# Optimization experiments

Hardware: AMD Instinct MI355X
Metric: run time of the kernel (lower is better)

The kernel has to match this reference:

```python
import jax, jax.numpy as jnp
import numpy as np

H = 1024   # hidden_dim
I = 256    # input_dim
T = 128    # time_step
NW = 4     # input_num (weeks)
N = 100    # stocks = 5 categories * 20
C, G = 5, 20


def gru(x, Wih, Whh, bih, bhh):
    """Torch-style single-layer GRU. x: (B,T,I) batch_first -> (B,T,H). Gate order r,z,n."""
    gx = jnp.einsum('bti,gi->btg', x, Wih) + bih  # (B,T,3H) input projections precomputed
    h0 = jnp.zeros((x.shape[0], Whh.shape[1]), x.dtype)

    def step(h, g):
        gh = h @ Whh.T + bhh
        xr, xz, xn = jnp.split(g, 3, axis=-1)
        hr, hz, hn = jnp.split(gh, 3, axis=-1)
        r = jax.nn.sigmoid(xr + hr)
        z = jax.nn.sigmoid(xz + hz)
        n = jnp.tanh(xn + r * hn)
        h = (1.0 - z) * n + z * h
        return h, h

    _, ys = jax.lax.scan(step, h0, jnp.swapaxes(gx, 0, 1))
    return jnp.swapaxes(ys, 0, 1)


def att_block(x, W, b):
    """AttentionBlock: x (B,T,D); Linear over time axis, softmax over time, weighted sum."""
    xt = jnp.swapaxes(x, 1, 2)                    # (B,D,T)
    probs = jax.nn.softmax(xt @ W.T + b, axis=-1) # (B,D,T)
    probs = jnp.swapaxes(probs, 1, 2)             # (B,T,D)
    return (probs * x).sum(axis=1)                # (B,D)


def gat(x, edges, W, a_s, a_d, bias):
    """PyG GATConv, heads=1, add_self_loops=True, leaky_relu slope 0.2."""
    n = x.shape[0]
    h = x @ W.T                                   # (n,H)
    loop = jnp.arange(n)
    src = jnp.concatenate([edges[0], loop])
    dst = jnp.concatenate([edges[1], loop])
    e = jax.nn.leaky_relu((h @ a_s)[src] + (h @ a_d)[dst], 0.2)
    m = jax.ops.segment_max(e, dst, num_segments=n)
    ex = jnp.exp(e - m[dst])
    s = jax.ops.segment_sum(ex, dst, num_segments=n)
    alpha = ex / s[dst]
    return jax.ops.segment_sum(alpha[:, None] * h[src], dst, num_segments=n) + bias


def setup_inputs() -> dict:
    key = jax.random.key(0)
    ks = iter(jax.random.split(key, 64))
    p = lambda *s: jax.random.normal(next(ks), s, dtype=jnp.float32) * 0.05
    inp = {}
    for i in range(NW):
        inp[f'w{i}'] = jax.random.normal(next(ks), (N, T, I), dtype=jnp.float32)
    inp['inner_edge'] = jax.random.randint(next(ks), (2, 2000), 0, N, dtype=jnp.int32)
    inp['outer_edge'] = jax.random.randint(next(ks), (2, 25), 0, C, dtype=jnp.int32)
    # per-week sequence encoders (stacked)
    inp['enc_Wih'] = p(NW, 3 * H, I); inp['enc_Whh'] = p(NW, 3 * H, H)
    inp['enc_bih'] = p(NW, 3 * H);    inp['enc_bhh'] = p(NW, 3 * H)
    inp['enc_attW'] = p(NW, T, T);    inp['enc_attb'] = p(NW, T)
    # weekly GRU (not batch_first in torch!)
    inp['wk_Wih'] = p(3 * H, H); inp['wk_Whh'] = p(3 * H, H)
    inp['wk_bih'] = p(3 * H);    inp['wk_bhh'] = p(3 * H)
    inp['wkatt_W'] = p(NW, NW); inp['wkatt_b'] = p(NW)
    inp['pool_W'] = p(G, G);    inp['pool_b'] = p(G)
    inp['ig_W'] = p(H, H); inp['ig_as'] = p(H); inp['ig_ad'] = p(H); inp['ig_b'] = p(H)
    inp['cg_W'] = p(H, H); inp['cg_as'] = p(H); inp['cg_ad'] = p(H); inp['cg_b'] = p(H)
    inp['fus_W'] = p(H, 3 * H); inp['fus_b'] = p(H)
    inp['reg_W'] = p(1, H); inp['reg_b'] = p(1)
    inp['cls_W'] = p(1, H); inp['cls_b'] = p(1)
    return inp


def reference(w0, w1, w2, w3, inner_edge, outer_edge,
              enc_Wih, enc_Whh, enc_bih, enc_bhh, enc_attW, enc_attb,
              wk_Wih, wk_Whh, wk_bih, wk_bhh, wkatt_W, wkatt_b,
              pool_W, pool_b, ig_W, ig_as, ig_ad, ig_b,
              cg_W, cg_as, cg_ad, cg_b, fus_W, fus_b,
              reg_W, reg_b, cls_W, cls_b):
    weeks = [w0, w1, w2, w3]
    embs = []
    for i in range(NW):
        seq = gru(weeks[i], enc_Wih[i], enc_Whh[i], enc_bih[i], enc_bhh[i])  # (N,T,H)
        embs.append(att_block(seq, enc_attW[i], enc_attb[i])[:, None, :])    # (N,1,H)
    we = jnp.concatenate(embs, axis=1)                                       # (N,NW,H)
    # torch nn.GRU default seq-major: scans over dim0 (N stocks), batch=NW
    we = jnp.swapaxes(gru(jnp.swapaxes(we, 0, 1), wk_Wih, wk_Whh, wk_bih, wk_bhh), 0, 1)
    wav = att_block(we, wkatt_W, wkatt_b)                                    # (N,H)
    inner = gat(wav, inner_edge, ig_W, ig_as, ig_ad, ig_b).reshape(C, G, -1)
    wav3 = wav.reshape(C, G, -1)
    cat = att_block(wav3, pool_W, pool_b)                                    # (C,H)
    cat = gat(cat, outer_edge, cg_W, cg_as, cg_ad, cg_b)                     # (C,H)
    cat = jnp.broadcast_to(cat[:, None, :], (C, G, cat.shape[-1]))
    f = jnp.concatenate([wav3, cat, inner], axis=-1)                         # (C,G,3H)
    f = jax.nn.relu(f @ fus_W.T + fus_b)
    reg = (f @ reg_W.T + reg_b).reshape(-1)
    cls = jax.nn.sigmoid(f @ cls_W.T + cls_b).reshape(-1)
    return reg, cls
```

## Files before the change

kernel.cpp:

```cpp
#include <hip/hip_runtime.h>
#include <hip/hip_bf16.h>

#define NW 4
#define NST 100
#define TT 128
#define II 256
#define HH 1024
#define H3 3072

typedef _Float16 h8 __attribute__((ext_vector_type(8)));
typedef float f4 __attribute__((ext_vector_type(4)));

__device__ __forceinline__ float sigf(float x) { return 1.0f / (1.0f + expf(-x)); }

__device__ __forceinline__ float4 ld_f4_sc1(const float* p) {
    union { unsigned long long u[2]; float4 v; } r;
    r.u[0] = __hip_atomic_load((unsigned long long*)p, __ATOMIC_RELAXED, __HIP_MEMORY_SCOPE_AGENT);
    r.u[1] = __hip_atomic_load((unsigned long long*)p + 1, __ATOMIC_RELAXED, __HIP_MEMORY_SCOPE_AGENT);
    return r.v;
}
__device__ __forceinline__ float ld_f_sc1(const float* p) {
    return __hip_atomic_load((float*)p, __ATOMIC_RELAXED, __HIP_MEMORY_SCOPE_AGENT);
}

__device__ __forceinline__ void spin_wait(unsigned* f, unsigned t) {
    int guard = 0;
    while (__hip_atomic_load(f, __ATOMIC_RELAXED, __HIP_MEMORY_SCOPE_AGENT) <= t) {
        __builtin_amdgcn_s_sleep(2);
        if (++guard > (1 << 20)) break;
    }
}

__global__ void zero_k(float* a, int n) {
    int i = blockIdx.x * 256 + threadIdx.x;
    if (i < n) a[i] = 0.0f;
}

__global__ void convW_k(const float* __restrict__ Whh, const float* __restrict__ Wih,
                        _Float16* __restrict__ Wc) {
    int col = blockIdx.x * 256 + threadIdx.x;
    int r = blockIdx.y;
    int w = blockIdx.z;
    float v = (col < HH) ? Whh[((size_t)w * H3 + r) * HH + col]
                         : Wih[((size_t)w * H3 + r) * II + (col - HH)];
    Wc[((size_t)w * H3 + r) * 1280 + col] = (_Float16)v;
}

__global__ void convWk_k(const float* __restrict__ src, _Float16* __restrict__ dst) {
    int col = blockIdx.x * 256 + threadIdx.x;
    int r = blockIdx.y;
    dst[(size_t)r * HH + col] = (_Float16)src[(size_t)r * HH + col];
}

__global__ void xcvt_k(const float* __restrict__ x0, const float* __restrict__ x1,
                       const float* __restrict__ x2, const float* __restrict__ x3,
                       _Float16* __restrict__ xT) {
    int idx = blockIdx.x * 256 + threadIdx.x;
    int k8 = idx & 31;
    int m  = (idx >> 5) & 127;
    int t  = (idx >> 12) & 127;
    int w  = idx >> 19;
    const float* xw = (w == 0) ? x0 : (w == 1) ? x1 : (w == 2) ? x2 : x3;
    h8 hv = {};
    if (m < NST) {
        const float* s = xw + ((size_t)m * TT + t) * II + k8 * 8;
        float4 fa = *(const float4*)s;
        float4 fb = *(const float4*)(s + 4);
        hv[0] = (_Float16)fa.x; hv[1] = (_Float16)fa.y;
        hv[2] = (_Float16)fa.z; hv[3] = (_Float16)fa.w;
        hv[4] = (_Float16)fb.x; hv[5] = (_Float16)fb.y;
        hv[6] = (_Float16)fb.z; hv[7] = (_Float16)fb.w;
    }
    *(h8*)&xT[(((size_t)w * TT + t) * 128 + m) * II + k8 * 8] = hv;
}

__global__ void wTcvt_k(const float* __restrict__ attW, float* __restrict__ wT) {
    int tp = threadIdx.x;
    int t  = blockIdx.x;
    int w  = blockIdx.y;
    wT[((size_t)w * TT + t) * TT + tp] = attW[((size_t)w * TT + tp) * TT + t];
}

__global__ void convB_k(const float* __restrict__ bih, const float* __restrict__ bhh,
                        float* __restrict__ bc) {
    int j = blockIdx.x * 256 + threadIdx.x;
    int w = blockIdx.y;
    const float* bi = bih + w * H3;
    const float* bh = bhh + w * H3;
    float* o = bc + w * 4096;
    o[j] = bi[j] + bh[j];
    o[1024 + j] = bi[1024 + j] + bh[1024 + j];
    o[2048 + j] = bi[2048 + j];
    o[3072 + j] = bh[2048 + j];
}

#define ENC_LDS_HALFS (40 * 48 * 40)
#define ENC_LDS_BYTES (ENC_LDS_HALFS * 2)

__global__ __launch_bounds__(256) void enc_fused_k(
    const _Float16* __restrict__ Wc, const float* __restrict__ bc,
    const _Float16* __restrict__ xT,
    _Float16* __restrict__ hhA, _Float16* __restrict__ hhB,
    _Float16* __restrict__ seq, unsigned* flags)
{
    extern __shared__ _Float16 Bs[];

    int id = blockIdx.x;
    int rr = id & 7, qq = id >> 3;
    int w  = rr >> 1;
    int bx = qq * 2 + (rr & 1);
    int j0 = bx * 16;

    const _Float16* Wcw = Wc + (size_t)w * H3 * 1280;
    const float* bcw = bc + w * 4096;
    _Float16* hA = hhA + (size_t)w * 128 * HH;
    _Float16* hB = hhB + (size_t)w * 128 * HH;
    unsigned* fw = flags + (size_t)w * 64 * 16;

    int tid = threadIdx.x;
    int lane = tid & 63, wi = tid >> 6, quad = lane >> 4, l15 = lane & 15;

    if (tid < 192) {
        int brow = tid >> 2, bseg = tid & 3;
        const _Float16* bsrc =
            Wcw + (size_t)((brow >> 4) * 1024 + j0 + (brow & 15)) * 1280 + bseg * 8;
        #pragma unroll 8
        for (int c = 0; c < 40; c++) {
            uint4 v = *(const uint4*)(bsrc + c * 32);
            *(uint4*)&Bs[((size_t)c * 48 + brow) * 40 + bseg * 8] = v;
        }
    }
    __syncthreads();

    int j = j0 + l15;
    float br = bcw[j], bz = bcw[1024 + j], bni = bcw[2048 + j], bnh = bcw[3072 + j];
    int r0 = wi * 32 + l15, r1 = wi * 32 + 16 + l15;
    float hreg[2][4] = {};

    for (int t = 0; t < TT; t++) {
        const _Float16* hin = (t & 1) ? hB : hA;
        _Float16* hout = (t & 1) ? hA : hB;
        const _Float16* xt = xT + ((size_t)w * TT + t) * 128 * II;
        const _Float16* pA0h = hin + (size_t)r0 * HH + quad * 8;
        const _Float16* pA1h = hin + (size_t)r1 * HH + quad * 8;
        const _Float16* pA0x = xt + (size_t)r0 * II + quad * 8;
        const _Float16* pA1x = xt + (size_t)r1 * II + quad * 8;

        f4 aR[2] = {}, aZ[2] = {}, aNH[2] = {}, aNX[2] = {};

        h8 rb0[8], rb1[8];
        #pragma unroll
        for (int u = 0; u < 8; u++) {
            rb0[u] = *(const h8*)(pA0h + u * 32);
            rb1[u] = *(const h8*)(pA1h + u * 32);
        }

        #pragma unroll 8
        for (int c = 0; c < 40; c++) {
            int u = c & 7;
            h8 a0 = rb0[u], a1 = rb1[u];
            int cn = c + 8;
            if (cn < 32) {
                rb0[u] = *(const h8*)(pA0h + cn * 32);
                rb1[u] = *(const h8*)(pA1h + cn * 32);
            } else if (cn < 40) {
                rb0[u] = *(const h8*)(pA0x + (cn - 32) * 32);
                rb1[u] = *(const h8*)(pA1x + (cn - 32) * 32);
            }
            const _Float16* bb = &Bs[(size_t)(c * 48) * 40];
            h8 bf0 = *(const h8*)&bb[l15 * 40 + quad * 8];
            h8 bf1 = *(const h8*)&bb[(16 + l15) * 40 + quad * 8];
            h8 bf2 = *(const h8*)&bb[(32 + l15) * 40 + quad * 8];
            aR[0] = __builtin_amdgcn_mfma_f32_16x16x32_f16(a0, bf0, aR[0], 0, 0, 0);
            aR[1] = __builtin_amdgcn_mfma_f32_16x16x32_f16(a1, bf0, aR[1], 0, 0, 0);
            aZ[0] = __builtin_amdgcn_mfma_f32_16x16x32_f16(a0, bf1, aZ[0], 0, 0, 0);
            aZ[1] = __builtin_amdgcn_mfma_f32_16x16x32_f16(a1, bf1, aZ[1], 0, 0, 0);
            if (c < 32) {
                aNH[0] = __builtin_amdgcn_mfma_f32_16x16x32_f16(a0, bf2, aNH[0], 0, 0, 0);
                aNH[1] = __builtin_amdgcn_mfma_f32_16x16x32_f16(a1, bf2, aNH[1], 0, 0, 0);
            } else {
                aNX[0] = __builtin_amdgcn_mfma_f32_16x16x32_f16(a0, bf2, aNX[0], 0, 0, 0);
                aNX[1] = __builtin_amdgcn_mfma_f32_16x16x32_f16(a1, bf2, aNX[1], 0, 0, 0);
            }
        }

        #pragma unroll
        for (int mi = 0; mi < 2; mi++) {
            #pragma unroll
            for (int p = 0; p < 4; p++) {
                int row = wi * 32 + mi * 16 + quad * 4 + p;
                float r = sigf(aR[mi][p] + br);
                float z = sigf(aZ[mi][p] + bz);
                float n = tanhf(aNX[mi][p] + bni + r * (aNH[mi][p] + bnh));
                float hv = (1.f - z) * n + z * hreg[mi][p];
                hreg[mi][p] = hv;
                unsigned short hb = __builtin_bit_cast(unsigned short, (_Float16)hv);
                unsigned ob = __shfl_xor((unsigned)hb, 1);
                unsigned pk = (unsigned)hb | (ob << 16);
                if (!(l15 & 1)) {
                    if (t < TT - 1)
                        __hip_atomic_store((unsigned*)&hout[(size_t)row * HH + j], pk,
                                           __ATOMIC_RELAXED, __HIP_MEMORY_SCOPE_AGENT);
                    if (row < NST)
                        __hip_atomic_store(
                            (unsigned*)&seq[(((size_t)w * NST + row) * TT + t) * HH + j], pk,
                            __ATOMIC_RELAXED, __HIP_MEMORY_SCOPE_AGENT);
                }
            }
        }
        if (t < TT - 1) {
            __syncthreads();
            if (tid == 0)
                __hip_atomic_store(&fw[bx * 16], (unsigned)(t + 1),
                                   __ATOMIC_RELAXED, __HIP_MEMORY_SCOPE_AGENT);
            if (tid < 64) spin_wait(&fw[tid * 16], (unsigned)t);
            __syncthreads();
            __builtin_amdgcn_fence(__ATOMIC_ACQUIRE, "agent");
        }
    }
}

__global__ __launch_bounds__(256) void att1_k(
    const _Float16* __restrict__ seq, const float* __restrict__ wT,
    const float* __restrict__ attb, float* __restrict__ wex)
{
    int d0 = blockIdx.x * 128;
    int n  = blockIdx.y;
    int w  = blockIdx.z;
    __shared__ _Float16 S[128][128];
    __shared__ float PM[16][136];
    int tid = threadIdx.x;
    const _Float16* sp = seq + ((size_t)(w * NST + n) * TT) * HH + d0;
    for (int q = tid; q < 2048; q += 256) {
        int t = q >> 4, seg = q & 15;
        *(h8*)&S[t][seg * 8] = *(const h8*)(sp + (size_t)t * HH + seg * 8);
    }
    __syncthreads();
    int tx = tid & 15, ty = tid >> 4;
    const float* Wg = wT + (size_t)w * TT * TT;
    float acc[8][8];
    #pragma unroll
    for (int i = 0; i < 8; i++) {
        float b = attb[w * TT + ty * 8 + i];
        for (int j = 0; j < 8; j++) acc[i][j] = b;
    }
    for (int t = 0; t < 128; t++) {
        float wv[8], sv[8];
        float4 wa = *(const float4*)&Wg[(size_t)t * TT + ty * 8];
        float4 wb = *(const float4*)&Wg[(size_t)t * TT + ty * 8 + 4];
        wv[0] = wa.x; wv[1] = wa.y; wv[2] = wa.z; wv[3] = wa.w;
        wv[4] = wb.x; wv[5] = wb.y; wv[6] = wb.z; wv[7] = wb.w;
        h8 s8 = *(const h8*)&S[t][tx * 8];
        #pragma unroll
        for (int j = 0; j < 8; j++) sv[j] = (float)s8[j];
        #pragma unroll
        for (int i = 0; i < 8; i++)
            #pragma unroll
            for (int j = 0; j < 8; j++) acc[i][j] += wv[i] * sv[j];
    }
    float cmax[8], csum[8];
    #pragma unroll
    for (int j = 0; j < 8; j++) {
        float m = acc[0][j];
        for (int i = 1; i < 8; i++) m = fmaxf(m, acc[i][j]);
        PM[ty][tx * 8 + j] = m;
    }
    __syncthreads();
    #pragma unroll
    for (int j = 0; j < 8; j++) {
        float m = -1e30f;
        for (int yy = 0; yy < 16; yy++) m = fmaxf(m, PM[yy][tx * 8 + j]);
        cmax[j] = m;
    }
    __syncthreads();
    #pragma unroll
    for (int j = 0; j < 8; j++) {
        float s = 0.f;
        for (int i = 0; i < 8; i++) { acc[i][j] = expf(acc[i][j] - cmax[j]); s += acc[i][j]; }
        PM[ty][tx * 8 + j] = s;
    }
    __syncthreads();
    #pragma unroll
    for (int j = 0; j < 8; j++) {
        float s = 0.f;
        for (int yy = 0; yy < 16; yy++) s += PM[yy][tx * 8 + j];
        csum[j] = s;
    }
    __syncthreads();
    #pragma unroll
    for (int i = 0; i < 8; i++) {
        h8 s8 = *(const h8*)&S[ty * 8 + i][tx * 8];
        #pragma unroll
        for (int j = 0; j < 8; j++) {
            if (i == 0) PM[ty][tx * 8 + j] = 0.f;
            PM[ty][tx * 8 + j] += acc[i][j] * (float)s8[j];
        }
    }
    __syncthreads();
    if (ty == 0) {
        #pragma unroll
        for (int j = 0; j < 8; j++) {
            float o = 0.f;
            for (int yy = 0; yy < 16; yy++) o += PM[yy][tx * 8 + j];
            wex[((size_t)w * NST + n) * HH + d0 + tx * 8 + j] = o / csum[j];
        }
    }
}

template <int RELU>
__global__ __launch_bounds__(256) void gemm_tn_k(
    const float* __restrict__ A, const float* __restrict__ B,
    const float* __restrict__ bias, float* __restrict__ C, int M, int N, int K)
{
    int n0 = blockIdx.x * 64, m0 = blockIdx.y * 64;
    __shared__ float As[16][64], Bs[16][64];
    int tid = threadIdx.x, tx = tid & 15, ty = tid >> 4;
    float acc[4][4] = {{0.f}};
    for (int k0 = 0; k0 < K; k0 += 16) {
        __syncthreads();
        for (int q = tid; q < 1024; q += 256) {
            int kk = q & 15, r = q >> 4;
            int m = m0 + r, nn = n0 + r;
            As[kk][r] = (m < M) ? A[(size_t)m * K + k0 + kk] : 0.f;
            Bs[kk][r] = (nn < N) ? B[(size_t)nn * K + k0 + kk] : 0.f;
        }
        __syncthreads();
        #pragma unroll
        for (int kk = 0; kk < 16; kk++) {
            float4 av = *(const float4*)&As[kk][ty * 4];
            float4 bv = *(const float4*)&Bs[kk][tx * 4];
            float a[4] = {av.x, av.y, av.z, av.w};
            float b[4] = {bv.x, bv.y, bv.z, bv.w};
            #pragma unroll
            for (int r = 0; r < 4; r++)
                #pragma unroll
                for (int c = 0; c < 4; c++) acc[r][c] += a[r] * b[c];
        }
    }
    #pragma unroll
    for (int r = 0; r < 4; r++) {
        int m = m0 + ty * 4 + r;
        if (m >= M) continue;
        #pragma unroll
        for (int c = 0; c < 4; c++) {
            int nn = n0 + tx * 4 + c;
            if (nn >= N) continue;
            float v = acc[r][c] + (bias ? bias[nn] : 0.f);
            if (RELU) v = fmaxf(v, 0.f);
            C[(size_t)m * N + nn] = v;
        }
    }
}

__global__ __launch_bounds__(256) void wk_fused_k(
    const float* __restrict__ gxw, const _Float16* __restrict__ wkW,
    const float* __restrict__ bhh, float* __restrict__ hA,
    float* __restrict__ hB, float* __restrict__ we2, unsigned* flags)
{
    int tid = threadIdx.x;
    int wi = tid >> 6, lane = tid & 63;
    int j = blockIdx.x * 4 + wi;
    int k0 = lane * 16;
    float wf[3][16];
    #pragma unroll
    for (int g = 0; g < 3; g++) {
        h8 wa = *(const h8*)&wkW[(size_t)(g * HH + j) * HH + k0];
        h8 wb = *(const h8*)&wkW[(size_t)(g * HH + j) * HH + k0 + 8];
        #pragma unroll
        for (int i = 0; i < 8; i++) { wf[g][i] = (float)wa[i]; wf[g][8 + i] = (float)wb[i]; }
    }
    float b0 = bhh[j], b1 = bhh[HH + j], b2 = bhh[2 * HH + j];

    for (int t = 0; t < NST; t++) {
        const float* hin = (t & 1) ? hB : hA;
        float* hout = (t & 1) ? hA : hB;
        float acc[4][3] = {};
        #pragma unroll
        for (int b = 0; b < 4; b++) {
            float hv[16];
            #pragma unroll
            for (int s = 0; s < 4; s++) {
                float4 hq = ld_f4_sc1(&hin[b * HH + k0 + s * 4]);
                hv[s * 4] = hq.x; hv[s * 4 + 1] = hq.y;
                hv[s * 4 + 2] = hq.z; hv[s * 4 + 3] = hq.w;
            }
            #pragma unroll
            for (int g = 0; g < 3; g++)
                #pragma unroll
                for (int i = 0; i < 16; i++) acc[b][g] += wf[g][i] * hv[i];
        }
        #pragma unroll
        for (int b = 0; b < 4; b++)
            #pragma unroll
            for (int g = 0; g < 3; g++)
                for (int o = 32; o; o >>= 1) acc[b][g] += __shfl_down(acc[b][g], o);
        if (lane == 0) {
            for (int b = 0; b < 4; b++) {
                const float* gx = gxw + ((size_t)b * NST + t) * H3;
                float hr = acc[b][0] + b0;
                float hz = acc[b][1] + b1;
                float hn = acc[b][2] + b2;
                float r = sigf(gx[j] + hr);
                float z = sigf(gx[HH + j] + hz);
                float n = tanhf(gx[2 * HH + j] + r * hn);
                float hv = (1.f - z) * n + z * ld_f_sc1(&hin[b * HH + j]);
                __hip_atomic_store(&hout[b * HH + j], hv,
                                   __ATOMIC_RELAXED, __HIP_MEMORY_SCOPE_AGENT);
                we2[((size_t)t * 4 + b) * HH + j] = hv;
            }
        }
        if (t < NST - 1) {
            __syncthreads();
            if (tid == 0)
                __hip_atomic_store(&flags[blockIdx.x * 16], (unsigned)(t + 1),
                                   __ATOMIC_RELAXED, __HIP_MEMORY_SCOPE_AGENT);
            spin_wait(&flags[tid * 16], (unsigned)t);
            __syncthreads();
        }
    }
}

__global__ void wkatt_k(const float* __restrict__ we2, const float* __restrict__ W,
                        const float* __restrict__ bv, float* __restrict__ wav)
{
    int n = blockIdx.x;
    for (int d = threadIdx.x; d < HH; d += 256) {
        float v[4], l[4];
        #pragma unroll
        for (int tp = 0; tp < 4; tp++) v[tp] = we2[((size_t)n * 4 + tp) * HH + d];
        float mx = -1e30f;
        #pragma unroll
        for (int tp = 0; tp < 4; tp++) {
            float s = bv[tp];
            for (int t2 = 0; t2 < 4; t2++) s += v[t2] * W[tp * 4 + t2];
            l[tp] = s; mx = fmaxf(mx, s);
        }
        float se = 0.f, o = 0.f;
        #pragma unroll
        for (int tp = 0; tp < 4; tp++) {
            float e = expf(l[tp] - mx);
            se += e; o += e * v[tp];
        }
        wav[(size_t)n * HH + d] = o / se;
    }
}

__global__ void poolatt_k(const float* __restrict__ wav, const float* __restrict__ W,
                          const float* __restrict__ bv, float* __restrict__ cat1)
{
    int c = blockIdx.x;
    for (int d = threadIdx.x; d < HH; d += 256) {
        float v[20], l[20];
        for (int t2 = 0; t2 < 20; t2++) v[t2] = wav[((size_t)c * 20 + t2) * HH + d];
        float mx = -1e30f;
        for (int tp = 0; tp < 20; tp++) {
            float s = bv[tp];
            for (int t2 = 0; t2 < 20; t2++) s += v[t2] * W[tp * 20 + t2];
            l[tp] = s; mx = fmaxf(mx, s);
        }
        float se = 0.f, o = 0.f;
        for (int tp = 0; tp < 20; tp++) {
            float e = expf(l[tp] - mx);
            se += e; o += e * v[tp];
        }
        cat1[(size_t)c * HH + d] = o / se;
    }
}

__global__ void gat_dots_k(const float* __restrict__ h, const float* __restrict__ as_,
                           const float* __restrict__ ad_, float* __restrict__ ss,
                           float* __restrict__ sd)
{
    int i = blockIdx.x, tid = threadIdx.x;
    float s1 = 0.f, s2 = 0.f;
    for (int k = tid; k < HH; k += 256) {
        float v = h[(size_t)i * HH + k];
        s1 += v * as_[k]; s2 += v * ad_[k];
    }
    __shared__ float r1[256], r2[256];
    r1[tid] = s1; r2[tid] = s2; __syncthreads();
    for (int s = 128; s; s >>= 1) {
        if (tid < s) { r1[tid] += r1[tid + s]; r2[tid] += r2[tid + s]; }
        __syncthreads();
    }
    if (tid == 0) { ss[i] = r1[0]; sd[i] = r2[0]; }
}

#define MAXE 256
__global__ __launch_bounds__(256) void gat_agg_k(
    const float* __restrict__ hmat, const int* __restrict__ esrc,
    const int* __restrict__ edst, int nedges, const float* __restrict__ ss,
    const float* __restrict__ sd, const float* __restrict__ bias, float* __restrict__ outp)
{
    int i = blockIdx.x, tid = threadIdx.x;
    __shared__ int cnt;
    __shared__ int msrc[MAXE];
    __shared__ float mw[MAXE];
    __shared__ float inv_s;
    if (tid == 0) {
        cnt = 1; msrc[0] = i;
        float e = ss[i] + sd[i];
        mw[0] = e > 0.f ? e : 0.2f * e;
    }
    __syncthreads();
    for (int e = tid; e < nedges; e += 256) {
        if (edst[e] == i) {
            int p = atomicAdd(&cnt, 1);
            if (p < MAXE) {
                int s = esrc[e];
                msrc[p] = s;
                float v = ss[s] + sd[i];
                mw[p] = v > 0.f ? v : 0.2f * v;
            }
        }
    }
    __syncthreads();
    int m = min(cnt, MAXE);
    if (tid == 0) {
        float mx = -1e30f;
        for (int p = 0; p < m; p++) mx = fmaxf(mx, mw[p]);
        float s = 0.f;
        for (int p = 0; p < m; p++) { float e = expf(mw[p] - mx); mw[p] = e; s += e; }
        inv_s = 1.0f / s;
    }
    __syncthreads();
    for (int d = tid; d < HH; d += 256) {
        float a = 0.f;
        for (int p = 0; p < m; p++) a += mw[p] * hmat[(size_t)msrc[p] * HH + d];
        outp[(size_t)i * HH + d] = a * inv_s + bias[d];
    }
}

__global__ void concat_k(const float* __restrict__ wav, const float* __restrict__ gc,
                         const float* __restrict__ gi, float* __restrict__ cc)
{
    int row = blockIdx.x;
    int c = row / 20;
    for (int k = threadIdx.x; k < H3; k += 256) {
        float v;
        if (k < HH) v = wav[(size_t)row * HH + k];
        else if (k < 2 * HH) v = gc[(size_t)c * HH + (k - HH)];
        else v = gi[(size_t)row * HH + (k - 2 * HH)];
        cc[(size_t)row * H3 + k] = v;
    }
}

__global__ void heads_k(const float* __restrict__ f, const float* __restrict__ regW,
                        const float* __restrict__ regb, const float* __restrict__ clsW,
                        const float* __restrict__ clsb, float* __restrict__ outp)
{
    int i = blockIdx.x, tid = threadIdx.x;
    float s1 = 0.f, s2 = 0.f;
    for (int k = tid; k < HH; k += 256) {
        float v = f[(size_t)i * HH + k];
        s1 += v * regW[k]; s2 += v * clsW[k];
    }
    __shared__ float r1[256], r2[256];
    r1[tid] = s1; r2[tid] = s2; __syncthreads();
    for (int s = 128; s; s >>= 1) {
        if (tid < s) { r1[tid] += r1[tid + s]; r2[tid] += r2[tid + s]; }
        __syncthreads();
    }
    if (tid == 0) {
        outp[i] = r1[0] + regb[0];
        outp[100 + i] = sigf(r2[0] + clsb[0]);
    }
}

extern "C" void kernel_launch(void* const* d_in, const int* in_sizes, int n_in,
                              void* d_out, int out_size, void* d_ws, size_t ws_size,
                              hipStream_t stream)
{
    (void)in_sizes; (void)n_in; (void)out_size; (void)ws_size;
    const float* x0 = (const float*)d_in[0];
    const float* x1 = (const float*)d_in[1];
    const float* x2 = (const float*)d_in[2];
    const float* x3 = (const float*)d_in[3];
    const int*   ie = (const int*)d_in[4];
    const int*   oe = (const int*)d_in[5];
    const float* enc_Wih = (const float*)d_in[6];
    const float* enc_Whh = (const float*)d_in[7];
    const float* enc_bih = (const float*)d_in[8];
    const float* enc_bhh = (const float*)d_in[9];
    const float* enc_attW = (const float*)d_in[10];
    const float* enc_attb = (const float*)d_in[11];
    const float* wk_Wih = (const float*)d_in[12];
    const float* wk_Whh = (const float*)d_in[13];
    const float* wk_bih = (const float*)d_in[14];
    const float* wk_bhh = (const float*)d_in[15];
    const float* wkatt_W = (const float*)d_in[16];
    const float* wkatt_b = (const float*)d_in[17];
    const float* pool_W = (const float*)d_in[18];
    const float* pool_b = (const float*)d_in[19];
    const float* ig_W = (const float*)d_in[20];
    const float* ig_as = (const float*)d_in[21];
    const float* ig_ad = (const float*)d_in[22];
    const float* ig_b = (const float*)d_in[23];
    const float* cg_W = (const float*)d_in[24];
    const float* cg_as = (const float*)d_in[25];
    const float* cg_ad = (const float*)d_in[26];
    const float* cg_b = (const float*)d_in[27];
    const float* fus_W = (const float*)d_in[28];
    const float* fus_b = (const float*)d_in[29];
    const float* reg_W = (const float*)d_in[30];
    const float* reg_b = (const float*)d_in[31];
    const float* cls_W = (const float*)d_in[32];
    const float* cls_b = (const float*)d_in[33];
    float* outp = (float*)d_out;

    char* p = (char*)d_ws;
    auto alloc = [&](size_t bytes) { char* r = p; p += (bytes + 255) & ~(size_t)255; return (void*)r; };
    unsigned* flags = (unsigned*)alloc(2 * 256 * 16 * 4);
    _Float16* Wcat = (_Float16*)alloc((size_t)NW * H3 * 1280 * 2);
    float* bc = (float*)alloc((size_t)NW * 4 * HH * 4);
    _Float16* wkW = (_Float16*)alloc((size_t)H3 * HH * 2);
    _Float16* xT = (_Float16*)alloc((size_t)NW * TT * 128 * II * 2);
    float* wT = (float*)alloc((size_t)NW * TT * TT * 4);
    _Float16* hhA = (_Float16*)alloc((size_t)NW * 128 * HH * 2);
    _Float16* hhB = (_Float16*)alloc((size_t)NW * 128 * HH * 2);
    _Float16* seq = (_Float16*)alloc((size_t)NW * NST * TT * HH * 2);
    float* wex = (float*)alloc((size_t)NW * NST * HH * 4);
    float* gxw = (float*)alloc((size_t)NW * NST * H3 * 4);
    float* hwA = (float*)alloc(4 * HH * 4);
    float* hwB = (float*)alloc(4 * HH * 4);
    float* we2 = (float*)alloc((size_t)NST * 4 * HH * 4);
    float* wav = (float*)alloc((size_t)NST * HH * 4);
    float* hi  = (float*)alloc((size_t)NST * HH * 4);
    float* si_s = (float*)alloc(128 * 4);
    float* si_d = (float*)alloc(128 * 4);
    float* gi  = (float*)alloc((size_t)NST * HH * 4);
    float* cat1 = (float*)alloc(5 * HH * 4);
    float* hc  = (float*)alloc(5 * HH * 4);
    float* sc_s = (float*)alloc(64 * 4);
    float* sc_d = (float*)alloc(64 * 4);
    float* gc  = (float*)alloc(5 * HH * 4);
    float* cc  = (float*)alloc((size_t)NST * H3 * 4);
    float* fbuf = (float*)alloc((size_t)NST * HH * 4);

    static bool attr_done = false;
    if (!attr_done) {
        hipFuncSetAttribute((const void*)enc_fused_k,
                            hipFuncAttributeMaxDynamicSharedMemorySize, ENC_LDS_BYTES);
        attr_done = true;
    }

    zero_k<<<32, 256, 0, stream>>>((float*)flags, 2 * 256 * 16);
    convW_k<<<dim3(5, H3, NW), 256, 0, stream>>>(enc_Whh, enc_Wih, Wcat);
    convB_k<<<dim3(4, NW), 256, 0, stream>>>(enc_bih, enc_bhh, bc);
    convWk_k<<<dim3(4, H3), 256, 0, stream>>>(wk_Whh, wkW);
    xcvt_k<<<8192, 256, 0, stream>>>(x0, x1, x2, x3, xT);
    wTcvt_k<<<dim3(TT, NW), 128, 0, stream>>>(enc_attW, wT);
    zero_k<<<(NW * 128 * HH / 2 + 255) / 256, 256, 0, stream>>>((float*)hhA, NW * 128 * HH / 2);
    zero_k<<<(4 * HH + 255) / 256, 256, 0, stream>>>(hwA, 4 * HH);

    enc_fused_k<<<256, 256, ENC_LDS_BYTES, stream>>>(
        Wcat, bc, xT, hhA, hhB, seq, flags);

    att1_k<<<dim3(8, NST, NW), 256, 0, stream>>>(seq, wT, enc_attb, wex);

    gemm_tn_k<0><<<dim3(48, 7), 256, 0, stream>>>(wex, wk_Wih, wk_bih, gxw, 400, H3, HH);

    wk_fused_k<<<256, 256, 0, stream>>>(gxw, wkW, wk_bhh, hwA, hwB, we2, flags + 256 * 16);

    wkatt_k<<<NST, 256, 0, stream>>>(we2, wkatt_W, wkatt_b, wav);

    gemm_tn_k<0><<<dim3(16, 2), 256, 0, stream>>>(wav, ig_W, nullptr, hi, NST, HH, HH);
    gat_dots_k<<<NST, 256, 0, stream>>>(hi, ig_as, ig_ad, si_s, si_d);
    gat_agg_k<<<NST, 256, 0, stream>>>(hi, ie, ie + 2000, 2000, si_s, si_d, ig_b, gi);

    poolatt_k<<<5, 256, 0, stream>>>(wav, pool_W, pool_b, cat1);
    gemm_tn_k<0><<<dim3(16, 1), 256, 0, stream>>>(cat1, cg_W, nullptr, hc, 5, HH, HH);
    gat_dots_k<<<5, 256, 0, stream>>>(hc, cg_as, cg_ad, sc_s, sc_d);
    gat_agg_k<<<5, 256, 0, stream>>>(hc, oe, oe + 25, 25, sc_s, sc_d, cg_b, gc);

    concat_k<<<NST, 256, 0, stream>>>(wav, gc, gi, cc);
    gemm_tn_k<1><<<dim3(16, 2), 256, 0, stream>>>(cc, fus_W, fus_b, fbuf, NST, HH, H3);
    heads_k<<<NST, 256, 0, stream>>>(fbuf, reg_W, reg_b, cls_W, cls_b, outp);
}
```

Measured before the change: 5.227 ms.

## Defer seq stores past flag publish, use atomic exchange, repack LDS layout

The encoder GRU kernel now stores the recurrent hidden state with atomic exchanges. It publishes the step flag before writing the seq output, so seq stores overlap other blocks' waiting rather than delaying the barrier. The weight tile in LDS is repacked from a padded 40-half stride to a dense 32-half per-gate layout, which may introduce bank conflicts but shrinks LDS use. The spin-wait sleep is shortened, and the week GRU also switches to an atomic exchange for its hidden-state stores, possibly to make those writes complete before the flag release.

```diff
diff --git a/kernel.cpp b/kernel.cpp
--- a/kernel.cpp
+++ b/kernel.cpp
@@ -26,8 +26,8 @@
 __device__ __forceinline__ void spin_wait(unsigned* f, unsigned t) {
     int guard = 0;
     while (__hip_atomic_load(f, __ATOMIC_RELAXED, __HIP_MEMORY_SCOPE_AGENT) <= t) {
-        __builtin_amdgcn_s_sleep(2);
-        if (++guard > (1 << 20)) break;
+        __builtin_amdgcn_s_sleep(1);
+        if (++guard > (1 << 21)) break;
     }
 }
 
@@ -94,7 +94,7 @@
     o[3072 + j] = bh[2048 + j];
 }
 
-#define ENC_LDS_HALFS (40 * 48 * 40)
+#define ENC_LDS_HALFS (40 * 3 * 16 * 32)
 #define ENC_LDS_BYTES (ENC_LDS_HALFS * 2)
 
 __global__ __launch_bounds__(256) void enc_fused_k(
@@ -122,12 +122,13 @@
 
     if (tid < 192) {
         int brow = tid >> 2, bseg = tid & 3;
+        int g = brow >> 4, jj = brow & 15;
         const _Float16* bsrc =
-            Wcw + (size_t)((brow >> 4) * 1024 + j0 + (brow & 15)) * 1280 + bseg * 8;
+            Wcw + (size_t)(g * 1024 + j0 + jj) * 1280 + bseg * 8;
         #pragma unroll 8
         for (int c = 0; c < 40; c++) {
             uint4 v = *(const uint4*)(bsrc + c * 32);
-            *(uint4*)&Bs[((size_t)c * 48 + brow) * 40 + bseg * 8] = v;
+            *(uint4*)&Bs[(((size_t)c * 3 + g) * 16 + jj) * 32 + bseg * 8] = v;
         }
     }
     __syncthreads();
@@ -167,10 +168,10 @@
                 rb0[u] = *(const h8*)(pA0x + (cn - 32) * 32);
                 rb1[u] = *(const h8*)(pA1x + (cn - 32) * 32);
             }
-            const _Float16* bb = &Bs[(size_t)(c * 48) * 40];
-            h8 bf0 = *(const h8*)&bb[l15 * 40 + quad * 8];
-            h8 bf1 = *(const h8*)&bb[(16 + l15) * 40 + quad * 8];
-            h8 bf2 = *(const h8*)&bb[(32 + l15) * 40 + quad * 8];
+            const _Float16* bb = &Bs[(size_t)c * 1536];
+            h8 bf0 = *(const h8*)&bb[l15 * 32 + quad * 8];
+            h8 bf1 = *(const h8*)&bb[512 + l15 * 32 + quad * 8];
+            h8 bf2 = *(const h8*)&bb[1024 + l15 * 32 + quad * 8];
             aR[0] = __builtin_amdgcn_mfma_f32_16x16x32_f16(a0, bf0, aR[0], 0, 0, 0);
             aR[1] = __builtin_amdgcn_mfma_f32_16x16x32_f16(a1, bf0, aR[1], 0, 0, 0);
             aZ[0] = __builtin_amdgcn_mfma_f32_16x16x32_f16(a0, bf1, aZ[0], 0, 0, 0);
@@ -184,6 +185,7 @@
             }
         }
 
+        unsigned pks[2][4];
         #pragma unroll
         for (int mi = 0; mi < 2; mi++) {
             #pragma unroll
@@ -197,15 +199,10 @@
                 unsigned short hb = __builtin_bit_cast(unsigned short, (_Float16)hv);
                 unsigned ob = __shfl_xor((unsigned)hb, 1);
                 unsigned pk = (unsigned)hb | (ob << 16);
-                if (!(l15 & 1)) {
-                    if (t < TT - 1)
-                        __hip_atomic_store((unsigned*)&hout[(size_t)row * HH + j], pk,
-                                           __ATOMIC_RELAXED, __HIP_MEMORY_SCOPE_AGENT);
-                    if (row < NST)
-                        __hip_atomic_store(
-                            (unsigned*)&seq[(((size_t)w * NST + row) * TT + t) * HH + j], pk,
-                            __ATOMIC_RELAXED, __HIP_MEMORY_SCOPE_AGENT);
-                }
+                pks[mi][p] = pk;
+                if (!(l15 & 1) && t < TT - 1)
+                    __hip_atomic_exchange((unsigned*)&hout[(size_t)row * HH + j], pk,
+                                          __ATOMIC_RELAXED, __HIP_MEMORY_SCOPE_AGENT);
             }
         }
         if (t < TT - 1) {
@@ -213,6 +210,19 @@
             if (tid == 0)
                 __hip_atomic_store(&fw[bx * 16], (unsigned)(t + 1),
                                    __ATOMIC_RELAXED, __HIP_MEMORY_SCOPE_AGENT);
+        }
+        #pragma unroll
+        for (int mi = 0; mi < 2; mi++) {
+            #pragma unroll
+            for (int p = 0; p < 4; p++) {
+                int row = wi * 32 + mi * 16 + quad * 4 + p;
+                if (!(l15 & 1) && row < NST)
+                    __hip_atomic_store(
+                        (unsigned*)&seq[(((size_t)w * NST + row) * TT + t) * HH + j],
+                        pks[mi][p], __ATOMIC_RELAXED, __HIP_MEMORY_SCOPE_AGENT);
+            }
+        }
+        if (t < TT - 1) {
             if (tid < 64) spin_wait(&fw[tid * 16], (unsigned)t);
             __syncthreads();
             __builtin_amdgcn_fence(__ATOMIC_ACQUIRE, "agent");
@@ -404,8 +414,8 @@
                 float z = sigf(gx[HH + j] + hz);
                 float n = tanhf(gx[2 * HH + j] + r * hn);
                 float hv = (1.f - z) * n + z * ld_f_sc1(&hin[b * HH + j]);
-                __hip_atomic_store(&hout[b * HH + j], hv,
-                                   __ATOMIC_RELAXED, __HIP_MEMORY_SCOPE_AGENT);
+                __hip_atomic_exchange(&hout[b * HH + j], hv,
+                                      __ATOMIC_RELAXED, __HIP_MEMORY_SCOPE_AGENT);
                 we2[((size_t)t * 4 + b) * HH + j] = hv;
             }
         }
```

Measured after the change: 5.142 ms. About the same (-1.6%).
